# Optimization experiments

Measured on AMD Instinct MI355X. Metric: run time of the kernel, lower is better.

## Reference

```python
import jax, jax.numpy as jnp
import numpy as np

E, EDIM, NDIM, H = 262144, 256, 256, 8
DH = NDIM // H
EPS = 1e-5  # torch nn.LayerNorm default


def _param(k, shape, scale=0.02):
    return jax.random.normal(k, shape, jnp.float32) * scale


def setup_inputs() -> dict:
    key = jax.random.key(0)
    ks = jax.random.split(key, 12)
    return {
        "x": jax.random.normal(ks[0], (E, EDIM), jnp.float32),
        "src_x": jax.random.normal(ks[1], (E, NDIM), jnp.float32),
        "dst_x": jax.random.normal(ks[2], (E, NDIM), jnp.float32),
        # multi-head cross-attention params (q from edge feats, k/v from node feats)
        "Wq": _param(ks[3], (EDIM, NDIM)), "bq": jnp.zeros((NDIM,), jnp.float32),
        "Wk": _param(ks[4], (NDIM, NDIM)), "bk": jnp.zeros((NDIM,), jnp.float32),
        "Wv": _param(ks[5], (NDIM, NDIM)), "bv": jnp.zeros((NDIM,), jnp.float32),
        "Wo": _param(ks[6], (NDIM, EDIM)), "bo": jnp.zeros((EDIM,), jnp.float32),
        "W1": _param(ks[7], (EDIM, 4 * EDIM)), "b1": jnp.zeros((4 * EDIM,), jnp.float32),
        "W2": _param(ks[8], (4 * EDIM, EDIM)), "b2": jnp.zeros((EDIM,), jnp.float32),
        # two LayerNorms
        "g1": jnp.ones((EDIM,), jnp.float32), "be1": jnp.zeros((EDIM,), jnp.float32),
        "g2": jnp.ones((EDIM,), jnp.float32), "be2": jnp.zeros((EDIM,), jnp.float32),
    }


def _layer_norm(h, g, b):
    m = jnp.mean(h, axis=-1, keepdims=True)
    v = jnp.mean(jnp.square(h - m), axis=-1, keepdims=True)
    return (h - m) * jax.lax.rsqrt(v + EPS) * g + b


def reference(x, src_x, dst_x, Wq, bq, Wk, bk, Wv, bv, Wo, bo,
              W1, b1, W2, b2, g1, be1, g2, be2):
    # per-edge cross-attention: query = edge feat (len 1), keys/values = (src, dst) (len 2)
    q = (x @ Wq + bq).reshape(E, H, DH)                 # [E,H,DH]
    kv = jnp.stack([src_x, dst_x], axis=1)              # [E,2,NDIM]
    k = (kv @ Wk + bk).reshape(E, 2, H, DH)
    v = (kv @ Wv + bv).reshape(E, 2, H, DH)
    scale = 1.0 / float(np.sqrt(DH))
    scores = jnp.einsum('ehd,ekhd->ehk', q, k) * scale  # [E,H,2]
    attn = jax.nn.softmax(scores, axis=-1)
    ctx = jnp.einsum('ehk,ekhd->ehd', attn, v).reshape(E, NDIM)
    out = ctx @ Wo + bo                                  # [E,EDIM]
    h = _layer_norm(x + out, g1, be1)
    ff = jax.nn.relu(h @ W1 + b1) @ W2 + b2
    return _layer_norm(h + ff, g2, be2)
```

## Files before the change

kernel.cpp:

```cpp
#include <hip/hip_runtime.h>
#include <hip/hip_bf16.h>
#include <math.h>

#define NROWS   262144
#define BM      64
#define THREADS 512
#define LDSB    (65536 + 2048)

using bf16x8 = __attribute__((ext_vector_type(8))) short;
using s16x4  = __attribute__((ext_vector_type(4))) short;
using f32x4  = __attribute__((ext_vector_type(4))) float;

__device__ __forceinline__ short f2bf(float f) {
  __hip_bfloat16 h = __float2bfloat16(f);
  return __builtin_bit_cast(short, h);
}
__device__ __forceinline__ float bf2f(short s) {
  __hip_bfloat16 h = __builtin_bit_cast(__hip_bfloat16, s);
  return __bfloat162float(h);
}
__device__ __forceinline__ int swz(int row, int col) {
  return row * 512 + ((col * 2) ^ ((row & 7) << 4));
}

__device__ __forceinline__ float red16(float p) {
  p += __shfl_xor(p, 1, 64);
  p += __shfl_xor(p, 2, 64);
  p += __shfl_xor(p, 4, 64);
  p += __shfl_xor(p, 8, 64);
  return p;
}

__device__ __forceinline__ void zero_acc(f32x4 (&acc)[4][2]) {
#pragma unroll
  for (int m = 0; m < 4; ++m)
#pragma unroll
    for (int n = 0; n < 2; ++n)
      acc[m][n] = (f32x4){0.f, 0.f, 0.f, 0.f};
}
__device__ __forceinline__ void zero_acc1(f32x4 (&acc)[4]) {
#pragma unroll
  for (int m = 0; m < 4; ++m)
    acc[m] = (f32x4){0.f, 0.f, 0.f, 0.f};
}

__device__ __forceinline__ void stage_tile(char* __restrict__ buf,
                                           const float* __restrict__ g, int tid) {
#pragma unroll 2
  for (int it = 0; it < 8; ++it) {
    int idx = it * THREADS + tid;
    int r = idx >> 6;
    int c = (idx & 63) << 2;
    float4 v = *(const float4*)(g + r * 256 + c);
    s16x4 o;
    o[0] = f2bf(v.x); o[1] = f2bf(v.y); o[2] = f2bf(v.z); o[3] = f2bf(v.w);
    *(s16x4*)(buf + swz(r, c)) = o;
  }
}

__device__ __forceinline__ void gemm256(const char* __restrict__ Abuf,
                                        const short* __restrict__ WT, int Kw,
                                        int cb, int koff, int li, int hi,
                                        f32x4 (&acc)[4][2]) {
  const short* w0 = WT + (size_t)(cb + li) * Kw + koff + hi * 8;
  const short* w1 = WT + (size_t)(cb + 16 + li) * Kw + koff + hi * 8;
#pragma unroll 2
  for (int kk = 0; kk < 256; kk += 32) {
    int ka = kk + hi * 8;
    bf16x8 b0 = *(const bf16x8*)(w0 + kk);
    bf16x8 b1 = *(const bf16x8*)(w1 + kk);
    bf16x8 a[4];
#pragma unroll
    for (int m = 0; m < 4; ++m)
      a[m] = *(const bf16x8*)(Abuf + swz(16 * m + li, ka));
#pragma unroll
    for (int m = 0; m < 4; ++m) {
      acc[m][0] = __builtin_amdgcn_mfma_f32_16x16x32_bf16(a[m], b0, acc[m][0], 0, 0, 0);
      acc[m][1] = __builtin_amdgcn_mfma_f32_16x16x32_bf16(a[m], b1, acc[m][1], 0, 0, 0);
    }
  }
}

__device__ __forceinline__ void gemm256_n(const char* __restrict__ Abuf,
                                          const short* __restrict__ WT, int Kw,
                                          int col0, int koff, int li, int hi,
                                          f32x4 (&acc)[4]) {
  const short* w0 = WT + (size_t)(col0 + li) * Kw + koff + hi * 8;
#pragma unroll 2
  for (int kk = 0; kk < 256; kk += 32) {
    int ka = kk + hi * 8;
    bf16x8 b0 = *(const bf16x8*)(w0 + kk);
    bf16x8 a[4];
#pragma unroll
    for (int m = 0; m < 4; ++m)
      a[m] = *(const bf16x8*)(Abuf + swz(16 * m + li, ka));
#pragma unroll
    for (int m = 0; m < 4; ++m)
      acc[m] = __builtin_amdgcn_mfma_f32_16x16x32_bf16(a[m], b0, acc[m], 0, 0, 0);
  }
}

__global__ void prep(const float* __restrict__ Wq, const float* __restrict__ Wk,
                     const float* __restrict__ Wv, const float* __restrict__ Wo,
                     const float* __restrict__ W1, const float* __restrict__ W2,
                     short* __restrict__ wt) {
  int idx = blockIdx.x * blockDim.x + threadIdx.x;
  if (idx < 262144) {
    int m = idx >> 16;
    const float* W = (m == 0) ? Wq : (m == 1) ? Wk : (m == 2) ? Wv : Wo;
    float s = (m == 0) ? 0.17677669529663687f : 1.0f;
    int l = idx & 65535;
    int n = l >> 8, k = l & 255;
    wt[idx] = f2bf(W[k * 256 + n] * s);
  } else if (idx < 524288) {
    int l = idx - 262144;
    int n = l >> 8, k = l & 255;
    wt[idx] = f2bf(W1[k * 1024 + n]);
  } else {
    int l = idx - 524288;
    int n = l >> 10, k = l & 1023;
    wt[idx] = f2bf(W2[k * 256 + n]);
  }
}

__global__ __attribute__((amdgpu_waves_per_eu(4, 4))) __launch_bounds__(THREADS)
void fused(const float* __restrict__ x, const float* __restrict__ sx,
           const float* __restrict__ dx,
           const float* __restrict__ bq,
           const float* __restrict__ bv, const float* __restrict__ bo,
           const float* __restrict__ b1, const float* __restrict__ b2,
           const float* __restrict__ g1, const float* __restrict__ be1,
           const float* __restrict__ g2, const float* __restrict__ be2,
           const short* __restrict__ wt, float* __restrict__ out) {
  extern __shared__ char sm[];
  char* Tbuf = sm;
  char* Cbuf = sm + 32768;
  float* sc    = (float*)(sm + 65536);
  float* scrT  = (float*)Tbuf;
  float* scr2T = (float*)(Tbuf + 4096);
  float* scrC  = (float*)Cbuf;
  float* scr2C = (float*)(Cbuf + 4096);

  const short* WqT = wt;
  const short* WkT = wt + 65536;
  const short* WvT = wt + 131072;
  const short* WoT = wt + 196608;
  const short* W1T = wt + 262144;
  const short* W2T = wt + 524288;

  const int tid  = threadIdx.x;
  const int w    = tid >> 6;
  const int lane = tid & 63;
  const int li   = lane & 15;
  const int hi   = lane >> 4;
  const int cb   = w * 32;
  const size_t row0 = (size_t)blockIdx.x * BM;

  const float* xt = x  + row0 * 256;
  const float* st = sx + row0 * 256;
  const float* dt = dx + row0 * 256;

  stage_tile(Tbuf, xt, tid);
  __syncthreads();

  f32x4 qa[4][2];
  zero_acc(qa);
  gemm256(Tbuf, WqT, 256, cb, 0, li, hi, qa);
  stage_tile(Cbuf, dt, tid);
  {
    const float scl = 0.17677669529663687f;
    float bq0 = bq[cb + li] * scl, bq1 = bq[cb + 16 + li] * scl;
#pragma unroll
    for (int m = 0; m < 4; ++m)
#pragma unroll
      for (int j = 0; j < 4; ++j) {
        qa[m][0][j] += bq0;
        qa[m][1][j] += bq1;
      }
  }
  __syncthreads();

  {
    float p[4][4];
#pragma unroll
    for (int m = 0; m < 4; ++m)
#pragma unroll
      for (int j = 0; j < 4; ++j) p[m][j] = 0.f;
#pragma unroll
    for (int nf = 0; nf < 2; ++nf) {
      f32x4 ka[4];
      zero_acc1(ka);
      gemm256_n(Cbuf, WkT, 256, cb + 16 * nf, 0, li, hi, ka);
#pragma unroll
      for (int m = 0; m < 4; ++m)
#pragma unroll
        for (int j = 0; j < 4; ++j) p[m][j] += qa[m][nf][j] * ka[m][j];
    }
    stage_tile(Tbuf, st, tid);
#pragma unroll
    for (int m = 0; m < 4; ++m)
#pragma unroll
      for (int j = 0; j < 4; ++j) {
        float pr = red16(p[m][j]);
        if (li == 0) sc[w * 64 + 16 * m + 4 * hi + j] = pr;
      }
  }
  __syncthreads();

  {
    float p[4][4];
#pragma unroll
    for (int m = 0; m < 4; ++m)
#pragma unroll
      for (int j = 0; j < 4; ++j) p[m][j] = 0.f;
#pragma unroll
    for (int nf = 0; nf < 2; ++nf) {
      f32x4 ka[4];
      zero_acc1(ka);
      gemm256_n(Tbuf, WkT, 256, cb + 16 * nf, 0, li, hi, ka);
#pragma unroll
      for (int m = 0; m < 4; ++m)
#pragma unroll
        for (int j = 0; j < 4; ++j) p[m][j] += qa[m][nf][j] * ka[m][j];
    }
#pragma unroll
    for (int m = 0; m < 4; ++m)
#pragma unroll
      for (int j = 0; j < 4; ++j) {
        float ps = red16(p[m][j]);
        int r = 16 * m + 4 * hi + j;
        float pdv = sc[w * 64 + r];
        float awv = 1.f / (1.f + expf(pdv - ps));
        if (li == 0) sc[w * 64 + r] = awv;
      }
  }
  f32x4 vs[4][2];
  zero_acc(vs);
  gemm256(Tbuf, WvT, 256, cb, 0, li, hi, vs);
#pragma unroll
  for (int nf = 0; nf < 2; ++nf) {
    f32x4 vd[4];
    zero_acc1(vd);
    gemm256_n(Cbuf, WvT, 256, cb + 16 * nf, 0, li, hi, vd);
    float bvn = bv[cb + 16 * nf + li];
#pragma unroll
    for (int m = 0; m < 4; ++m)
#pragma unroll
      for (int j = 0; j < 4; ++j) {
        float a = sc[w * 64 + 16 * m + 4 * hi + j];
        vs[m][nf][j] = a * vs[m][nf][j] + (1.f - a) * vd[m][j] + bvn;
      }
  }
  __syncthreads();

#pragma unroll
  for (int m = 0; m < 4; ++m)
#pragma unroll
    for (int n = 0; n < 2; ++n)
#pragma unroll
      for (int j = 0; j < 4; ++j)
        *(short*)(Cbuf + swz(16 * m + 4 * hi + j, cb + 16 * n + li)) = f2bf(vs[m][n][j]);
  __syncthreads();

  f32x4 oa[4][2];
  zero_acc(oa);
  gemm256(Cbuf, WoT, 256, cb, 0, li, hi, oa);
  {
    float bo0 = bo[cb + li], bo1 = bo[cb + 16 + li];
#pragma unroll
    for (int m = 0; m < 4; ++m)
#pragma unroll
      for (int j = 0; j < 4; ++j) {
        int r = 16 * m + 4 * hi + j;
        float v0 = oa[m][0][j] + bo0 + xt[r * 256 + cb + li];
        float v1 = oa[m][1][j] + bo1 + xt[r * 256 + cb + 16 + li];
        oa[m][0][j] = v0; oa[m][1][j] = v1;
        float s = red16(v0 + v1);
        float q = red16(v0 * v0 + v1 * v1);
        if (li == 0) { scrT[(w * 64 + r) * 2] = s; scrT[(w * 64 + r) * 2 + 1] = q; }
      }
  }
  __syncthreads();
  if (tid < BM) {
    float S = 0.f, Q = 0.f;
#pragma unroll
    for (int ww = 0; ww < 8; ++ww) {
      S += scrT[(ww * 64 + tid) * 2];
      Q += scrT[(ww * 64 + tid) * 2 + 1];
    }
    float mean = S * (1.f / 256.f);
    float var  = Q * (1.f / 256.f) - mean * mean;
    scr2T[tid * 2] = mean;
    scr2T[tid * 2 + 1] = rsqrtf(var + 1e-5f);
  }
  __syncthreads();
  {
    float g10 = g1[cb + li], g11 = g1[cb + 16 + li];
    float a10 = be1[cb + li], a11 = be1[cb + 16 + li];
#pragma unroll
    for (int m = 0; m < 4; ++m)
#pragma unroll
      for (int j = 0; j < 4; ++j) {
        int r = 16 * m + 4 * hi + j;
        float mean = scr2T[r * 2], rs = scr2T[r * 2 + 1];
        *(short*)(Cbuf + swz(r, cb + li))      = f2bf((oa[m][0][j] - mean) * rs * g10 + a10);
        *(short*)(Cbuf + swz(r, cb + 16 + li)) = f2bf((oa[m][1][j] - mean) * rs * g11 + a11);
      }
  }
  __syncthreads();

  f32x4 a2[4][2];
  zero_acc(a2);
#pragma unroll 1
  for (int c = 0; c < 4; ++c) {
#pragma unroll
    for (int nf = 0; nf < 2; ++nf) {
      f32x4 a1[4];
      zero_acc1(a1);
      gemm256_n(Cbuf, W1T, 256, 256 * c + cb + 16 * nf, 0, li, hi, a1);
      float b1n = b1[256 * c + cb + 16 * nf + li];
#pragma unroll
      for (int m = 0; m < 4; ++m)
#pragma unroll
        for (int j = 0; j < 4; ++j) {
          int r = 16 * m + 4 * hi + j;
          *(short*)(Tbuf + swz(r, cb + 16 * nf + li)) = f2bf(fmaxf(a1[m][j] + b1n, 0.f));
        }
    }
    __syncthreads();
    gemm256(Tbuf, W2T, 1024, cb, 256 * c, li, hi, a2);
    __syncthreads();
  }

  {
    float b20 = b2[cb + li], b21 = b2[cb + 16 + li];
#pragma unroll
    for (int m = 0; m < 4; ++m)
#pragma unroll
      for (int j = 0; j < 4; ++j) {
        int r = 16 * m + 4 * hi + j;
        a2[m][0][j] += b20 + bf2f(*(short*)(Cbuf + swz(r, cb + li)));
        a2[m][1][j] += b21 + bf2f(*(short*)(Cbuf + swz(r, cb + 16 + li)));
      }
  }
  __syncthreads();

#pragma unroll
  for (int m = 0; m < 4; ++m)
#pragma unroll
    for (int j = 0; j < 4; ++j) {
      int r = 16 * m + 4 * hi + j;
      float v0 = a2[m][0][j], v1 = a2[m][1][j];
      float s = red16(v0 + v1);
      float q = red16(v0 * v0 + v1 * v1);
      if (li == 0) { scrC[(w * 64 + r) * 2] = s; scrC[(w * 64 + r) * 2 + 1] = q; }
    }
  __syncthreads();
  if (tid < BM) {
    float S = 0.f, Q = 0.f;
#pragma unroll
    for (int ww = 0; ww < 8; ++ww) {
      S += scrC[(ww * 64 + tid) * 2];
      Q += scrC[(ww * 64 + tid) * 2 + 1];
    }
    float mean = S * (1.f / 256.f);
    float var  = Q * (1.f / 256.f) - mean * mean;
    scr2C[tid * 2] = mean;
    scr2C[tid * 2 + 1] = rsqrtf(var + 1e-5f);
  }
  __syncthreads();

  {
    float g20 = g2[cb + li], g21 = g2[cb + 16 + li];
    float a20 = be2[cb + li], a21 = be2[cb + 16 + li];
    float* orow = out + row0 * 256;
#pragma unroll
    for (int hf = 0; hf < 2; ++hf) {
#pragma unroll
      for (int m2 = 0; m2 < 2; ++m2) {
        int m = 2 * hf + m2;
#pragma unroll
        for (int j = 0; j < 4; ++j) {
          int r = 16 * m + 4 * hi + j;
          float mean = scr2C[r * 2], rs = scr2C[r * 2 + 1];
          int rr = r - 32 * hf;
          *(float*)(Tbuf + rr * 1024 + (((cb + li) * 4) ^ ((rr & 7) << 4)))
              = (a2[m][0][j] - mean) * rs * g20 + a20;
          *(float*)(Tbuf + rr * 1024 + (((cb + 16 + li) * 4) ^ ((rr & 7) << 4)))
              = (a2[m][1][j] - mean) * rs * g21 + a21;
        }
      }
      __syncthreads();
#pragma unroll
      for (int t = 0; t < 4; ++t) {
        int idx = t * THREADS + tid;
        int r = idx >> 6, c4 = idx & 63;
        f32x4 v = *(f32x4*)(Tbuf + r * 1024 + ((c4 * 16) ^ ((r & 7) << 4)));
        *(f32x4*)(orow + (hf * 32 + r) * 256 + c4 * 4) = v;
      }
      __syncthreads();
    }
  }
}

extern "C" void kernel_launch(void* const* d_in, const int* in_sizes, int n_in,
                              void* d_out, int out_size, void* d_ws, size_t ws_size,
                              hipStream_t stream) {
  const float* x   = (const float*)d_in[0];
  const float* sx  = (const float*)d_in[1];
  const float* dx  = (const float*)d_in[2];
  const float* Wq  = (const float*)d_in[3];
  const float* bq  = (const float*)d_in[4];
  const float* Wk  = (const float*)d_in[5];
  const float* Wv  = (const float*)d_in[7];
  const float* bv  = (const float*)d_in[8];
  const float* Wo  = (const float*)d_in[9];
  const float* bo  = (const float*)d_in[10];
  const float* W1  = (const float*)d_in[11];
  const float* b1  = (const float*)d_in[12];
  const float* W2  = (const float*)d_in[13];
  const float* b2  = (const float*)d_in[14];
  const float* g1  = (const float*)d_in[15];
  const float* be1 = (const float*)d_in[16];
  const float* g2  = (const float*)d_in[17];
  const float* be2 = (const float*)d_in[18];
  short* wt = (short*)d_ws;

  prep<<<dim3(1536), dim3(512), 0, stream>>>(Wq, Wk, Wv, Wo, W1, W2, wt);
  fused<<<dim3(NROWS / BM), dim3(THREADS), LDSB, stream>>>(
      x, sx, dx, bq, bv, bo, b1, b2, g1, be1, g2, be2, wt, (float*)d_out);
}
```

Baseline: 1.197 ms.

## Split fused kernel into attention+LN1 and FFN+LN2 kernels via bf16 buffer

The single fused kernel is split in two. The first does attention and LayerNorm1 and writes h as bf16 to a workspace buffer; the second reads h back and runs the FFN and LayerNorm2. Each kernel has smaller register and LDS needs and is built with launch_bounds(512,4), which should allow higher occupancy. It also stages the next input tile earlier to overlap loads with the GEMMs. The cost is an extra 128MB round trip through global memory and one more kernel launch, and the path only runs when the workspace is large enough.

```diff
diff --git a/kernel.cpp b/kernel.cpp
--- a/kernel.cpp
+++ b/kernel.cpp
@@ -5,7 +5,9 @@
 #define NROWS   262144
 #define BM      64
 #define THREADS 512
-#define LDSB    (65536 + 2048)
+#define LDSB_F  (65536 + 2048)
+#define LDSB_A  (65536 + 2048)
+#define LDSB_B  65536
 
 using bf16x8 = __attribute__((ext_vector_type(8))) short;
 using s16x4  = __attribute__((ext_vector_type(4))) short;
@@ -123,6 +125,326 @@
   }
 }
 
+__global__ __launch_bounds__(THREADS, 4)
+void attn_ln1(const float* __restrict__ x, const float* __restrict__ sx,
+              const float* __restrict__ dx,
+              const float* __restrict__ bq, const float* __restrict__ bv,
+              const float* __restrict__ bo,
+              const float* __restrict__ g1, const float* __restrict__ be1,
+              const short* __restrict__ wt, short* __restrict__ hout) {
+  extern __shared__ char sm[];
+  char* Tbuf = sm;
+  char* Cbuf = sm + 32768;
+  float* sc    = (float*)(sm + 65536);
+  float* scrT  = (float*)Tbuf;
+  float* scr2T = (float*)(Tbuf + 4096);
+
+  const short* WqT = wt;
+  const short* WkT = wt + 65536;
+  const short* WvT = wt + 131072;
+  const short* WoT = wt + 196608;
+
+  const int tid  = threadIdx.x;
+  const int w    = tid >> 6;
+  const int lane = tid & 63;
+  const int li   = lane & 15;
+  const int hi   = lane >> 4;
+  const int cb   = w * 32;
+  const size_t row0 = (size_t)blockIdx.x * BM;
+
+  const float* xt = x  + row0 * 256;
+  const float* st = sx + row0 * 256;
+  const float* dt = dx + row0 * 256;
+
+  stage_tile(Tbuf, xt, tid);
+  __syncthreads();
+
+  f32x4 qa[4][2];
+  zero_acc(qa);
+  stage_tile(Cbuf, dt, tid);
+  gemm256(Tbuf, WqT, 256, cb, 0, li, hi, qa);
+  {
+    const float scl = 0.17677669529663687f;
+    float bq0 = bq[cb + li] * scl, bq1 = bq[cb + 16 + li] * scl;
+#pragma unroll
+    for (int m = 0; m < 4; ++m)
+#pragma unroll
+      for (int j = 0; j < 4; ++j) {
+        qa[m][0][j] += bq0;
+        qa[m][1][j] += bq1;
+      }
+  }
+  __syncthreads();
+
+  {
+    stage_tile(Tbuf, st, tid);
+    float p[4][4];
+#pragma unroll
+    for (int m = 0; m < 4; ++m)
+#pragma unroll
+      for (int j = 0; j < 4; ++j) p[m][j] = 0.f;
+#pragma unroll
+    for (int nf = 0; nf < 2; ++nf) {
+      f32x4 ka[4];
+      zero_acc1(ka);
+      gemm256_n(Cbuf, WkT, 256, cb + 16 * nf, 0, li, hi, ka);
+#pragma unroll
+      for (int m = 0; m < 4; ++m)
+#pragma unroll
+        for (int j = 0; j < 4; ++j) p[m][j] += qa[m][nf][j] * ka[m][j];
+    }
+#pragma unroll
+    for (int m = 0; m < 4; ++m)
+#pragma unroll
+      for (int j = 0; j < 4; ++j) {
+        float pr = red16(p[m][j]);
+        if (li == 0) sc[w * 64 + 16 * m + 4 * hi + j] = pr;
+      }
+  }
+  __syncthreads();
+
+  {
+    float p[4][4];
+#pragma unroll
+    for (int m = 0; m < 4; ++m)
+#pragma unroll
+      for (int j = 0; j < 4; ++j) p[m][j] = 0.f;
+#pragma unroll
+    for (int nf = 0; nf < 2; ++nf) {
+      f32x4 ka[4];
+      zero_acc1(ka);
+      gemm256_n(Tbuf, WkT, 256, cb + 16 * nf, 0, li, hi, ka);
+#pragma unroll
+      for (int m = 0; m < 4; ++m)
+#pragma unroll
+        for (int j = 0; j < 4; ++j) p[m][j] += qa[m][nf][j] * ka[m][j];
+    }
+#pragma unroll
+    for (int m = 0; m < 4; ++m)
+#pragma unroll
+      for (int j = 0; j < 4; ++j) {
+        float ps = red16(p[m][j]);
+        int r = 16 * m + 4 * hi + j;
+        float pdv = sc[w * 64 + r];
+        float awv = 1.f / (1.f + expf(pdv - ps));
+        if (li == 0) sc[w * 64 + r] = awv;
+      }
+  }
+  f32x4 vs[4][2];
+  zero_acc(vs);
+  gemm256(Tbuf, WvT, 256, cb, 0, li, hi, vs);
+#pragma unroll
+  for (int nf = 0; nf < 2; ++nf) {
+    f32x4 vd[4];
+    zero_acc1(vd);
+    gemm256_n(Cbuf, WvT, 256, cb + 16 * nf, 0, li, hi, vd);
+    float bvn = bv[cb + 16 * nf + li];
+#pragma unroll
+    for (int m = 0; m < 4; ++m)
+#pragma unroll
+      for (int j = 0; j < 4; ++j) {
+        float a = sc[w * 64 + 16 * m + 4 * hi + j];
+        vs[m][nf][j] = a * vs[m][nf][j] + (1.f - a) * vd[m][j] + bvn;
+      }
+  }
+  __syncthreads();
+
+#pragma unroll
+  for (int m = 0; m < 4; ++m)
+#pragma unroll
+    for (int n = 0; n < 2; ++n)
+#pragma unroll
+      for (int j = 0; j < 4; ++j)
+        *(short*)(Cbuf + swz(16 * m + 4 * hi + j, cb + 16 * n + li)) = f2bf(vs[m][n][j]);
+  __syncthreads();
+
+  f32x4 oa[4][2];
+  zero_acc(oa);
+  gemm256(Cbuf, WoT, 256, cb, 0, li, hi, oa);
+  {
+    float bo0 = bo[cb + li], bo1 = bo[cb + 16 + li];
+#pragma unroll
+    for (int m = 0; m < 4; ++m)
+#pragma unroll
+      for (int j = 0; j < 4; ++j) {
+        int r = 16 * m + 4 * hi + j;
+        float v0 = oa[m][0][j] + bo0 + xt[r * 256 + cb + li];
+        float v1 = oa[m][1][j] + bo1 + xt[r * 256 + cb + 16 + li];
+        oa[m][0][j] = v0; oa[m][1][j] = v1;
+        float s = red16(v0 + v1);
+        float q = red16(v0 * v0 + v1 * v1);
+        if (li == 0) { scrT[(w * 64 + r) * 2] = s; scrT[(w * 64 + r) * 2 + 1] = q; }
+      }
+  }
+  __syncthreads();
+  if (tid < BM) {
+    float S = 0.f, Q = 0.f;
+#pragma unroll
+    for (int ww = 0; ww < 8; ++ww) {
+      S += scrT[(ww * 64 + tid) * 2];
+      Q += scrT[(ww * 64 + tid) * 2 + 1];
+    }
+    float mean = S * (1.f / 256.f);
+    float var  = Q * (1.f / 256.f) - mean * mean;
+    scr2T[tid * 2] = mean;
+    scr2T[tid * 2 + 1] = rsqrtf(var + 1e-5f);
+  }
+  __syncthreads();
+  {
+    float g10 = g1[cb + li], g11 = g1[cb + 16 + li];
+    float a10 = be1[cb + li], a11 = be1[cb + 16 + li];
+#pragma unroll
+    for (int m = 0; m < 4; ++m)
+#pragma unroll
+      for (int j = 0; j < 4; ++j) {
+        int r = 16 * m + 4 * hi + j;
+        float mean = scr2T[r * 2], rs = scr2T[r * 2 + 1];
+        *(short*)(Cbuf + swz(r, cb + li))      = f2bf((oa[m][0][j] - mean) * rs * g10 + a10);
+        *(short*)(Cbuf + swz(r, cb + 16 + li)) = f2bf((oa[m][1][j] - mean) * rs * g11 + a11);
+      }
+  }
+  __syncthreads();
+
+  {
+    short* hrow = hout + row0 * 256;
+#pragma unroll
+    for (int t = 0; t < 4; ++t) {
+      int idx = t * THREADS + tid;
+      int r = idx >> 5, c16 = idx & 31;
+      bf16x8 v = *(bf16x8*)(Cbuf + r * 512 + ((c16 * 16) ^ ((r & 7) << 4)));
+      *(bf16x8*)(hrow + r * 256 + c16 * 8) = v;
+    }
+  }
+}
+
+__global__ __launch_bounds__(THREADS, 4)
+void ffn_ln2(const short* __restrict__ hin, const float* __restrict__ b1,
+             const float* __restrict__ b2,
+             const float* __restrict__ g2, const float* __restrict__ be2,
+             const short* __restrict__ wt, float* __restrict__ out) {
+  extern __shared__ char sm[];
+  char* Cbuf = sm;
+  char* Tbuf = sm + 32768;
+  float* scrC  = (float*)Cbuf;
+  float* scr2C = (float*)(Cbuf + 4096);
+
+  const short* W1T = wt + 262144;
+  const short* W2T = wt + 524288;
+
+  const int tid  = threadIdx.x;
+  const int w    = tid >> 6;
+  const int lane = tid & 63;
+  const int li   = lane & 15;
+  const int hi   = lane >> 4;
+  const int cb   = w * 32;
+  const size_t row0 = (size_t)blockIdx.x * BM;
+
+  {
+    const short* hrow = hin + row0 * 256;
+#pragma unroll
+    for (int t = 0; t < 4; ++t) {
+      int idx = t * THREADS + tid;
+      int r = idx >> 5, c16 = idx & 31;
+      bf16x8 v = *(const bf16x8*)(hrow + r * 256 + c16 * 8);
+      *(bf16x8*)(Cbuf + r * 512 + ((c16 * 16) ^ ((r & 7) << 4))) = v;
+    }
+  }
+  __syncthreads();
+
+  f32x4 a2[4][2];
+  zero_acc(a2);
+#pragma unroll 1
+  for (int c = 0; c < 4; ++c) {
+#pragma unroll
+    for (int nf = 0; nf < 2; ++nf) {
+      f32x4 a1[4];
+      zero_acc1(a1);
+      gemm256_n(Cbuf, W1T, 256, 256 * c + cb + 16 * nf, 0, li, hi, a1);
+      float b1n = b1[256 * c + cb + 16 * nf + li];
+#pragma unroll
+      for (int m = 0; m < 4; ++m)
+#pragma unroll
+        for (int j = 0; j < 4; ++j) {
+          int r = 16 * m + 4 * hi + j;
+          *(short*)(Tbuf + swz(r, cb + 16 * nf + li)) = f2bf(fmaxf(a1[m][j] + b1n, 0.f));
+        }
+    }
+    __syncthreads();
+    gemm256(Tbuf, W2T, 1024, cb, 256 * c, li, hi, a2);
+    __syncthreads();
+  }
+
+  {
+    float b20 = b2[cb + li], b21 = b2[cb + 16 + li];
+#pragma unroll
+    for (int m = 0; m < 4; ++m)
+#pragma unroll
+      for (int j = 0; j < 4; ++j) {
+        int r = 16 * m + 4 * hi + j;
+        a2[m][0][j] += b20 + bf2f(*(short*)(Cbuf + swz(r, cb + li)));
+        a2[m][1][j] += b21 + bf2f(*(short*)(Cbuf + swz(r, cb + 16 + li)));
+      }
+  }
+  __syncthreads();
+
+#pragma unroll
+  for (int m = 0; m < 4; ++m)
+#pragma unroll
+    for (int j = 0; j < 4; ++j) {
+      int r = 16 * m + 4 * hi + j;
+      float v0 = a2[m][0][j], v1 = a2[m][1][j];
+      float s = red16(v0 + v1);
+      float q = red16(v0 * v0 + v1 * v1);
+      if (li == 0) { scrC[(w * 64 + r) * 2] = s; scrC[(w * 64 + r) * 2 + 1] = q; }
+    }
+  __syncthreads();
+  if (tid < BM) {
+    float S = 0.f, Q = 0.f;
+#pragma unroll
+    for (int ww = 0; ww < 8; ++ww) {
+      S += scrC[(ww * 64 + tid) * 2];
+      Q += scrC[(ww * 64 + tid) * 2 + 1];
+    }
+    float mean = S * (1.f / 256.f);
+    float var  = Q * (1.f / 256.f) - mean * mean;
+    scr2C[tid * 2] = mean;
+    scr2C[tid * 2 + 1] = rsqrtf(var + 1e-5f);
+  }
+  __syncthreads();
+
+  {
+    float g20 = g2[cb + li], g21 = g2[cb + 16 + li];
+    float a20 = be2[cb + li], a21 = be2[cb + 16 + li];
+    float* orow = out + row0 * 256;
+#pragma unroll
+    for (int hf = 0; hf < 2; ++hf) {
+#pragma unroll
+      for (int m2 = 0; m2 < 2; ++m2) {
+        int m = 2 * hf + m2;
+#pragma unroll
+        for (int j = 0; j < 4; ++j) {
+          int r = 16 * m + 4 * hi + j;
+          float mean = scr2C[r * 2], rs = scr2C[r * 2 + 1];
+          int rr = r - 32 * hf;
+          *(float*)(Tbuf + rr * 1024 + (((cb + li) * 4) ^ ((rr & 7) << 4)))
+              = (a2[m][0][j] - mean) * rs * g20 + a20;
+          *(float*)(Tbuf + rr * 1024 + (((cb + 16 + li) * 4) ^ ((rr & 7) << 4)))
+              = (a2[m][1][j] - mean) * rs * g21 + a21;
+        }
+      }
+      __syncthreads();
+#pragma unroll
+      for (int t = 0; t < 4; ++t) {
+        int idx = t * THREADS + tid;
+        int r = idx >> 6, c4 = idx & 63;
+        f32x4 v = *(f32x4*)(Tbuf + r * 1024 + ((c4 * 16) ^ ((r & 7) << 4)));
+        *(f32x4*)(orow + (hf * 32 + r) * 256 + c4 * 4) = v;
+      }
+      __syncthreads();
+    }
+  }
+}
+
 __global__ __attribute__((amdgpu_waves_per_eu(4, 4))) __launch_bounds__(THREADS)
 void fused(const float* __restrict__ x, const float* __restrict__ sx,
            const float* __restrict__ dx,
@@ -173,10 +495,7 @@
 #pragma unroll
     for (int m = 0; m < 4; ++m)
 #pragma unroll
-      for (int j = 0; j < 4; ++j) {
-        qa[m][0][j] += bq0;
-        qa[m][1][j] += bq1;
-      }
+      for (int j = 0; j < 4; ++j) { qa[m][0][j] += bq0; qa[m][1][j] += bq1; }
   }
   __syncthreads();
 
@@ -425,8 +744,18 @@
   const float* g2  = (const float*)d_in[17];
   const float* be2 = (const float*)d_in[18];
   short* wt = (short*)d_ws;
+  short* hbuf = wt + 786432;
+
+  const size_t need = 786432ULL * 2 + (size_t)NROWS * 256 * 2;
 
   prep<<<dim3(1536), dim3(512), 0, stream>>>(Wq, Wk, Wv, Wo, W1, W2, wt);
-  fused<<<dim3(NROWS / BM), dim3(THREADS), LDSB, stream>>>(
-      x, sx, dx, bq, bv, bo, b1, b2, g1, be1, g2, be2, wt, (float*)d_out);
-}
+  if (ws_size >= need) {
+    attn_ln1<<<dim3(NROWS / BM), dim3(THREADS), LDSB_A, stream>>>(
+        x, sx, dx, bq, bv, bo, g1, be1, wt, hbuf);
+    ffn_ln2<<<dim3(NROWS / BM), dim3(THREADS), LDSB_B, stream>>>(
+        hbuf, b1, b2, g2, be2, wt, (float*)d_out);
+  } else {
+    fused<<<dim3(NROWS / BM), dim3(THREADS), LDSB_F, stream>>>(
+        x, sx, dx, bq, bv, bo, b1, b2, g1, be1, g2, be2, wt, (float*)d_out);
+  }
+}
```

After: 1.187 ms. About the same (-0.9%).
